# Optimization experiments

Measured on AMD Instinct MI355X. Metric: run time of the kernel, lower is better.

The kernel has to match this reference:

```python
import jax, jax.numpy as jnp
import numpy as np

NUM_NODES = 32768  # B*N = 16*2048
NUM_REL = 10
NUM_BASES = 4
D = 256
E = 524288


def _rgcn_layer(x, src, dst, rel, basis, comp, root, bias):
    """Basis-decomposed relational GCN layer with per-relation mean aggregation.
    x: [N, Din], basis: [NB, Din, Dout], comp: [R, NB], root: [Din, Dout], bias: [Dout].
    """
    n = x.shape[0]
    # project all nodes through each basis once: [N, NB, Dout]
    xb = jnp.einsum('ni,bio->nbo', x, basis)
    coeff = comp[rel]  # [E, NB] per-edge basis coefficients
    # mean normalization per (destination node, relation) pair
    seg = rel * n + dst  # combined segment id, [E]
    cnt = jax.ops.segment_sum(jnp.ones(rel.shape[0], x.dtype), seg,
                              num_segments=NUM_REL * n)
    inv = jnp.where(cnt > 0, 1.0 / cnt, 0.0)[seg]  # [E]
    # per-edge message: sum_b coeff[e,b] * xb[src_e, b, :] (loop over small NB)
    msg = jnp.zeros((rel.shape[0], basis.shape[2]), x.dtype)
    for b in range(basis.shape[0]):
        msg = msg + coeff[:, b:b + 1] * xb[src, b]
    msg = msg * inv[:, None]
    agg = jax.ops.segment_sum(msg, dst, num_segments=n)  # [N, Dout]
    return agg + x @ root + bias


def setup_inputs() -> dict:
    key = jax.random.key(0)
    ks = jax.random.split(key, 16)
    p = lambda k, shp: (jax.random.normal(k, shp, jnp.float32) * 0.05)
    inp = {
        'x': jax.random.normal(ks[0], (16, 2048, D), jnp.float32),
        't': jax.random.randint(ks[1], (16,), 0, 1000),
        'obj_cond': jax.random.randint(ks[2], (16, 2048), 0, 160),
        'edge_cond': jax.random.randint(ks[3], (2, E), 0, NUM_NODES),
        'relation_cond': jax.random.randint(ks[4], (E,), 0, NUM_REL),
        # layer 0: 256 -> 256 (hidden)
        'basis0': p(ks[5], (NUM_BASES, D, D)),
        'comp0': p(ks[6], (NUM_REL, NUM_BASES)),
        'root0': p(ks[7], (D, D)),
        'bias0': p(ks[8], (D,)),
        # layer 1: 256 -> 256 (output)
        'basis1': p(ks[9], (NUM_BASES, D, D)),
        'comp1': p(ks[10], (NUM_REL, NUM_BASES)),
        'root1': p(ks[11], (D, D)),
        'bias1': p(ks[12], (D,)),
    }
    return inp


def reference(x, t, obj_cond, edge_cond, relation_cond,
              basis0, comp0, root0, bias0, basis1, comp1, root1, bias1):
    B, N, Dm = x.shape
    h = x.reshape(B * N, Dm)
    src, dst = edge_cond[0], edge_cond[1]
    h = _rgcn_layer(h, src, dst, relation_cond, basis0, comp0, root0, bias0)
    h = jax.nn.relu(h)  # hidden-layer activation (dropout disabled at eval)
    h = _rgcn_layer(h, src, dst, relation_cond, basis1, comp1, root1, bias1)
    return h.reshape(B, N, Dm)
```

## Files before the change

kernel.cpp:

```cpp
#include <hip/hip_runtime.h>
#include <stdint.h>

#define NNODES 32768
#define NREL 10
#define NBASES 4
#define DIM 256
#define NEDGE 524288
#define KW 1280
#define KBASE 1024

#define HB 2048
#define CB 8192
#define WB 80

typedef __attribute__((ext_vector_type(8))) short bf16x8;
typedef __attribute__((ext_vector_type(4))) float f32x4;
typedef __attribute__((ext_vector_type(2))) float f32x2;

__device__ __forceinline__ float bf2f(unsigned short u){
  union { unsigned int i; float f; } v; v.i = ((unsigned int)u) << 16; return v.f;
}
__device__ __forceinline__ float asf(unsigned int u){
  union { unsigned int i; float f; } v; v.i = u; return v.f;
}
__device__ __forceinline__ unsigned short f2bf(float f){
  union { float f; unsigned int i; } v; v.f = f;
  unsigned int x = v.i;
  unsigned int r = (x + 0x7FFFu + ((x >> 16) & 1u)) >> 16;
  return (unsigned short)r;
}
__device__ __forceinline__ void gll16(const void* g, void* l){
  __builtin_amdgcn_global_load_lds((const __attribute__((address_space(1))) void*)g,
                                   (__attribute__((address_space(3))) void*)l, 16, 0, 0);
}

__global__ __launch_bounds__(256) void mega_prep(
    const int* __restrict__ ec, const int* __restrict__ rel,
    int* __restrict__ cnt_rd,
    const float* __restrict__ x, unsigned short* __restrict__ Xh,
    const float* __restrict__ basis0, const float* __restrict__ root0,
    unsigned short* __restrict__ Wt0,
    const float* __restrict__ basis1, const float* __restrict__ root1,
    unsigned short* __restrict__ Wt1)
{
  __shared__ float tile[64][65];
  int bid = blockIdx.x;
  int t = threadIdx.x;
  if (bid < HB){
    int e = bid * 256 + t;
    int d = ec[NEDGE + e];
    int r = rel[e];
    atomicAdd(&cnt_rd[(r << 15) + d], 1);
  } else if (bid < HB + CB){
    int i = (bid - HB) * 256 + t;
    float4 v = ((const float4*)x)[i];
    ushort4 o; o.x = f2bf(v.x); o.y = f2bf(v.y); o.z = f2bf(v.z); o.w = f2bf(v.w);
    ((ushort4*)Xh)[i] = o;
  } else {
    int b = bid - HB - CB;
    int layer = b / WB; b %= WB;
    const float* basis = layer ? basis1 : basis0;
    const float* root  = layer ? root1  : root0;
    unsigned short* Wt = layer ? Wt1    : Wt0;
    int k0 = (b % 20) * 64;
    int n0 = (b / 20) * 64;
    int tn = t & 63, tk = t >> 6;
#pragma unroll
    for (int i = 0; i < 64; i += 4){
      int k = k0 + tk + i;
      float v = (k < KBASE) ? basis[(size_t)k * 256 + n0 + tn]
                            : root[(size_t)(k - KBASE) * 256 + n0 + tn];
      tile[tk + i][tn] = v;
    }
    __syncthreads();
#pragma unroll
    for (int i = 0; i < 64; i += 4){
      int n = n0 + tk + i;
      Wt[(size_t)n * KW + k0 + tn] = f2bf(tile[tn][tk + i]);
    }
  }
}

__global__ __launch_bounds__(1024) void scan1(const int* __restrict__ cnt_rd,
                                              int* __restrict__ offs, int* __restrict__ blksum)
{
  __shared__ int sh[1024];
  int tid = threadIdx.x; int gid = blockIdx.x * 1024 + tid;
  int v = 0;
#pragma unroll
  for (int r = 0; r < NREL; r++) v += cnt_rd[(r << 15) + gid];
  sh[tid] = v; __syncthreads();
  for (int off = 1; off < 1024; off <<= 1){
    int t = (tid >= off) ? sh[tid - off] : 0;
    __syncthreads(); sh[tid] += t; __syncthreads();
  }
  offs[gid] = sh[tid] - v;
  if (tid == 1023) blksum[blockIdx.x] = sh[1023];
}
__global__ __launch_bounds__(64) void scan2(int* __restrict__ blksum)
{
  __shared__ int sh[64];
  int tid = threadIdx.x;
  int v = (tid < NNODES / 1024) ? blksum[tid] : 0;
  sh[tid] = v; __syncthreads();
  for (int off = 1; off < 64; off <<= 1){
    int t = (tid >= off) ? sh[tid - off] : 0;
    __syncthreads(); sh[tid] += t; __syncthreads();
  }
  if (tid < NNODES / 1024) blksum[tid] = sh[tid] - v;
}
__global__ __launch_bounds__(1024) void scan3(int* __restrict__ offs, const int* __restrict__ blksum)
{
  int gid = blockIdx.x * 1024 + threadIdx.x;
  offs[gid] += blksum[blockIdx.x];
  if (gid == 0) offs[NNODES] = NEDGE;
}

__global__ void scatter_kernel(const int* __restrict__ ec, const int* __restrict__ rel,
                               const int* __restrict__ offs, int* __restrict__ cursor,
                               unsigned int* __restrict__ meta)
{
  int e = blockIdx.x * 256 + threadIdx.x;
  int s = ec[e];
  int d = ec[NEDGE + e];
  int r = rel[e];
  int p = offs[d] + atomicAdd(&cursor[d], 1);
  meta[p] = ((unsigned int)s << 4) | (unsigned int)r;
}

__global__ __launch_bounds__(256) void agg8(
    const unsigned short* __restrict__ Xin,
    const int* __restrict__ offs,
    const unsigned int* __restrict__ meta,
    const float* __restrict__ comp,
    const int* __restrict__ cnt_rd,
    unsigned short* __restrict__ z)
{
  __shared__ __attribute__((aligned(16))) float wtab[4][40];
  int t = threadIdx.x;
  int wv = t >> 6, lane = t & 63;
  int d = blockIdx.x * 4 + wv;
  if (lane < 40){
    int r = lane >> 2, b = lane & 3;
    int cnt = cnt_rd[(r << 15) + d];
    wtab[wv][lane] = (cnt > 0) ? comp[r * NBASES + b] / (float)cnt : 0.0f;
  }
  __syncthreads();

  const float4* wt4 = (const float4*)&wtab[wv][0];
  const char* Xb = (const char*)Xin;
  unsigned colb = (unsigned)(lane * 8);

  f32x2 acc[NBASES][2];
#pragma unroll
  for (int b = 0; b < NBASES; b++){ acc[b][0] = (f32x2){0.f,0.f}; acc[b][1] = (f32x2){0.f,0.f}; }

  int e0 = offs[d], e1 = offs[d + 1];
  int e = e0;

  for (; e + 7 < e1; e += 8){
    unsigned int m[8];
#pragma unroll
    for (int i = 0; i < 8; i++) m[i] = meta[e + i];
    uint2 v[8];
#pragma unroll
    for (int i = 0; i < 8; i++){
      unsigned off = ((m[i] & 0xFFFFFFF0u) << 5) + colb;
      v[i] = *(const uint2*)(Xb + off);
    }
#pragma unroll
    for (int i = 0; i < 8; i++){
      float4 w = wt4[m[i] & 15u];
      f32x2 f01, f23;
      f01.x = asf(v[i].x << 16); f01.y = asf(v[i].x & 0xffff0000u);
      f23.x = asf(v[i].y << 16); f23.y = asf(v[i].y & 0xffff0000u);
      acc[0][0] += (f32x2){w.x, w.x} * f01;  acc[0][1] += (f32x2){w.x, w.x} * f23;
      acc[1][0] += (f32x2){w.y, w.y} * f01;  acc[1][1] += (f32x2){w.y, w.y} * f23;
      acc[2][0] += (f32x2){w.z, w.z} * f01;  acc[2][1] += (f32x2){w.z, w.z} * f23;
      acc[3][0] += (f32x2){w.w, w.w} * f01;  acc[3][1] += (f32x2){w.w, w.w} * f23;
    }
  }

  for (; e < e1; e += 4){
    unsigned int m[4];
    float4 w[4];
#pragma unroll
    for (int i = 0; i < 4; i++){
      int ei = e + i;
      bool ok = ei < e1;
      m[i] = meta[ok ? ei : e1 - 1];
      float4 ww = wt4[m[i] & 15u];
      if (!ok){ ww.x = 0.f; ww.y = 0.f; ww.z = 0.f; ww.w = 0.f; }
      w[i] = ww;
    }
    uint2 v[4];
#pragma unroll
    for (int i = 0; i < 4; i++){
      unsigned off = ((m[i] & 0xFFFFFFF0u) << 5) + colb;
      v[i] = *(const uint2*)(Xb + off);
    }
#pragma unroll
    for (int i = 0; i < 4; i++){
      f32x2 f01, f23;
      f01.x = asf(v[i].x << 16); f01.y = asf(v[i].x & 0xffff0000u);
      f23.x = asf(v[i].y << 16); f23.y = asf(v[i].y & 0xffff0000u);
      acc[0][0] += (f32x2){w[i].x, w[i].x} * f01;  acc[0][1] += (f32x2){w[i].x, w[i].x} * f23;
      acc[1][0] += (f32x2){w[i].y, w[i].y} * f01;  acc[1][1] += (f32x2){w[i].y, w[i].y} * f23;
      acc[2][0] += (f32x2){w[i].z, w[i].z} * f01;  acc[2][1] += (f32x2){w[i].z, w[i].z} * f23;
      acc[3][0] += (f32x2){w[i].w, w[i].w} * f01;  acc[3][1] += (f32x2){w[i].w, w[i].w} * f23;
    }
  }

#pragma unroll
  for (int b = 0; b < NBASES; b++){
    ushort4 o;
    o.x = f2bf(acc[b][0].x); o.y = f2bf(acc[b][0].y);
    o.z = f2bf(acc[b][1].x); o.w = f2bf(acc[b][1].y);
    *(ushort4*)(z + (size_t)d * KBASE + b * 256 + lane * 4) = o;
  }
}

__global__ __launch_bounds__(256) void gemm4(
    const unsigned short* __restrict__ A0,
    const unsigned short* __restrict__ A1,
    const unsigned short* __restrict__ Wt,
    const float* __restrict__ bias,
    unsigned short* __restrict__ outh,
    float* __restrict__ outf,
    int mode)
{
  __shared__ __attribute__((aligned(16))) short As[64 * 32];
  __shared__ __attribute__((aligned(16))) short Bs[256 * 32];
  int tid  = threadIdx.x;
  int m0   = blockIdx.x * 64;
  int lane = tid & 63;
  int wn   = tid >> 6;
  int lq = lane >> 4, lr = lane & 15;

  f32x4 zero = {0.f, 0.f, 0.f, 0.f};
  f32x4 acc[4][4];
#pragma unroll
  for (int i = 0; i < 4; i++)
#pragma unroll
    for (int j = 0; j < 4; j++) acc[i][j] = zero;

  int arow = tid >> 2;
  int akc  = ((tid & 3) - (tid >> 3)) & 3;

  for (int k0 = 0; k0 < KW; k0 += 32){
    __syncthreads();
    {
      const unsigned short* ga;
      if (k0 < KBASE) ga = A0 + (size_t)(m0 + arow) * KBASE + k0 + akc * 8;
      else            ga = A1 + (size_t)(m0 + arow) * 256 + (k0 - KBASE) + akc * 8;
      gll16(ga, As + tid * 8);
    }
#pragma unroll
    for (int i = 0; i < 4; i++){
      int gb  = tid + i * 256;
      int row = gb >> 2;
      int kc  = ((gb & 3) - (gb >> 3)) & 3;
      gll16(Wt + (size_t)row * KW + k0 + kc * 8, Bs + gb * 8);
    }
    __syncthreads();

    bf16x8 af[4], bfr[4];
#pragma unroll
    for (int i = 0; i < 4; i++){
      int row = i * 16 + lr;
      af[i] = *(const bf16x8*)(As + row * 32 + (((lq + (row >> 1)) & 3) * 8));
    }
#pragma unroll
    for (int j = 0; j < 4; j++){
      int row = wn * 64 + j * 16 + lr;
      bfr[j] = *(const bf16x8*)(Bs + row * 32 + (((lq + (row >> 1)) & 3) * 8));
    }
#pragma unroll
    for (int i = 0; i < 4; i++)
#pragma unroll
      for (int j = 0; j < 4; j++)
        acc[i][j] = __builtin_amdgcn_mfma_f32_16x16x32_bf16(af[i], bfr[j], acc[i][j], 0, 0, 0);
  }

#pragma unroll
  for (int i = 0; i < 4; i++)
#pragma unroll
    for (int j = 0; j < 4; j++)
#pragma unroll
      for (int r = 0; r < 4; r++){
        int gm = m0 + i * 16 + lq * 4 + r;
        int gn = wn * 64 + j * 16 + lr;
        float v = acc[i][j][r] + bias[gn];
        size_t idx = (size_t)gm * 256 + gn;
        if (mode == 1) outh[idx] = f2bf(fmaxf(v, 0.f));
        else           outf[idx] = v;
      }
}

extern "C" void kernel_launch(void* const* d_in, const int* in_sizes, int n_in,
                              void* d_out, int out_size, void* d_ws, size_t ws_size,
                              hipStream_t stream)
{
  const float* x      = (const float*)d_in[0];
  const int*   ec     = (const int*)d_in[3];
  const int*   rel    = (const int*)d_in[4];
  const float* basis0 = (const float*)d_in[5];
  const float* comp0  = (const float*)d_in[6];
  const float* root0  = (const float*)d_in[7];
  const float* bias0  = (const float*)d_in[8];
  const float* basis1 = (const float*)d_in[9];
  const float* comp1  = (const float*)d_in[10];
  const float* root1  = (const float*)d_in[11];
  const float* bias1  = (const float*)d_in[12];

  char* p = (char*)d_ws;
  unsigned short* z   = (unsigned short*)p; p += (size_t)NNODES * KBASE * 2;
  unsigned short* Xh  = (unsigned short*)p; p += (size_t)NNODES * DIM * 2;
  unsigned short* h   = (unsigned short*)p; p += (size_t)NNODES * DIM * 2;
  unsigned short* Wt0 = (unsigned short*)p; p += (size_t)256 * KW * 2;
  unsigned short* Wt1 = (unsigned short*)p; p += (size_t)256 * KW * 2;
  unsigned int* meta  = (unsigned int*)p;   p += (size_t)NEDGE * 4;
  int* cnt_rd  = (int*)p;   p += (size_t)NREL * NNODES * 4;
  int* cursor  = (int*)p;   p += (size_t)NNODES * 4;
  int* offs    = (int*)p;   p += (size_t)(NNODES + 1) * 4;
  int* blksum  = (int*)p;   p += 1024;

  hipMemsetAsync(cnt_rd, 0, ((size_t)NREL * NNODES + (size_t)NNODES) * 4, stream);

  mega_prep<<<HB + CB + 2 * WB, 256, 0, stream>>>(
      ec, rel, cnt_rd, x, Xh, basis0, root0, Wt0, basis1, root1, Wt1);

  scan1<<<NNODES / 1024, 1024, 0, stream>>>(cnt_rd, offs, blksum);
  scan2<<<1, 64, 0, stream>>>(blksum);
  scan3<<<NNODES / 1024, 1024, 0, stream>>>(offs, blksum);
  scatter_kernel<<<NEDGE / 256, 256, 0, stream>>>(ec, rel, offs, cursor, meta);

  agg8<<<NNODES / 4, 256, 0, stream>>>(Xh, offs, meta, comp0, cnt_rd, z);
  gemm4<<<NNODES / 64, 256, 0, stream>>>(z, Xh, Wt0, bias0, h, nullptr, 1);

  agg8<<<NNODES / 4, 256, 0, stream>>>(h, offs, meta, comp1, cnt_rd, z);
  gemm4<<<NNODES / 64, 256, 0, stream>>>(z, h, Wt1, bias1, nullptr, (float*)d_out, 2);
}
```

Baseline: 322.8 us.

## Load GEMM weight fragments directly to registers and merge scan passes

After: 352.0 us. +9.1%, slower.

```diff
diff --git a/kernel.cpp b/kernel.cpp
--- a/kernel.cpp
+++ b/kernel.cpp
@@ -97,22 +97,19 @@
   offs[gid] = sh[tid] - v;
   if (tid == 1023) blksum[blockIdx.x] = sh[1023];
 }
-__global__ __launch_bounds__(64) void scan2(int* __restrict__ blksum)
-{
-  __shared__ int sh[64];
-  int tid = threadIdx.x;
-  int v = (tid < NNODES / 1024) ? blksum[tid] : 0;
-  sh[tid] = v; __syncthreads();
-  for (int off = 1; off < 64; off <<= 1){
-    int t = (tid >= off) ? sh[tid - off] : 0;
-    __syncthreads(); sh[tid] += t; __syncthreads();
-  }
-  if (tid < NNODES / 1024) blksum[tid] = sh[tid] - v;
-}
-__global__ __launch_bounds__(1024) void scan3(int* __restrict__ offs, const int* __restrict__ blksum)
-{
-  int gid = blockIdx.x * 1024 + threadIdx.x;
-  offs[gid] += blksum[blockIdx.x];
+__global__ __launch_bounds__(1024) void scan3b(int* __restrict__ offs, const int* __restrict__ blksum)
+{
+  __shared__ int pre;
+  int bid = blockIdx.x;
+  if (threadIdx.x < 64){
+    int v = ((int)threadIdx.x < bid && threadIdx.x < 32) ? blksum[threadIdx.x] : 0;
+#pragma unroll
+    for (int o = 1; o < 64; o <<= 1) v += __shfl_xor(v, o);
+    if (threadIdx.x == 0) pre = v;
+  }
+  __syncthreads();
+  int gid = bid * 1024 + threadIdx.x;
+  offs[gid] += pre;
   if (gid == 0) offs[NNODES] = NEDGE;
 }
 
@@ -220,7 +217,7 @@
   }
 }
 
-__global__ __launch_bounds__(256) void gemm4(
+__global__ __launch_bounds__(256) void gemm8(
     const unsigned short* __restrict__ A0,
     const unsigned short* __restrict__ A1,
     const unsigned short* __restrict__ Wt,
@@ -229,8 +226,7 @@
     float* __restrict__ outf,
     int mode)
 {
-  __shared__ __attribute__((aligned(16))) short As[64 * 32];
-  __shared__ __attribute__((aligned(16))) short Bs[256 * 32];
+  __shared__ __attribute__((aligned(16))) short As[64 * 64];
   int tid  = threadIdx.x;
   int m0   = blockIdx.x * 64;
   int lane = tid & 63;
@@ -244,42 +240,56 @@
 #pragma unroll
     for (int j = 0; j < 4; j++) acc[i][j] = zero;
 
-  int arow = tid >> 2;
-  int akc  = ((tid & 3) - (tid >> 3)) & 3;
-
-  for (int k0 = 0; k0 < KW; k0 += 32){
+  int arow0 = tid >> 3;
+  int akc0  = ((tid & 7) - (tid >> 4)) & 7;
+  int g1    = tid + 256;
+  int arow1 = g1 >> 3;
+  int akc1  = ((g1 & 7) - (g1 >> 4)) & 7;
+
+  const unsigned short* wtb[4];
+#pragma unroll
+  for (int j = 0; j < 4; j++)
+    wtb[j] = Wt + (size_t)(wn * 64 + j * 16 + lr) * KW + lq * 8;
+
+  for (int k0 = 0; k0 < KW; k0 += 64){
     __syncthreads();
     {
-      const unsigned short* ga;
-      if (k0 < KBASE) ga = A0 + (size_t)(m0 + arow) * KBASE + k0 + akc * 8;
-      else            ga = A1 + (size_t)(m0 + arow) * 256 + (k0 - KBASE) + akc * 8;
-      gll16(ga, As + tid * 8);
-    }
-#pragma unroll
-    for (int i = 0; i < 4; i++){
-      int gb  = tid + i * 256;
-      int row = gb >> 2;
-      int kc  = ((gb & 3) - (gb >> 3)) & 3;
-      gll16(Wt + (size_t)row * KW + k0 + kc * 8, Bs + gb * 8);
-    }
+      const unsigned short* ga0, *ga1;
+      if (k0 < KBASE){
+        ga0 = A0 + (size_t)(m0 + arow0) * KBASE + k0 + akc0 * 8;
+        ga1 = A0 + (size_t)(m0 + arow1) * KBASE + k0 + akc1 * 8;
+      } else {
+        ga0 = A1 + (size_t)(m0 + arow0) * 256 + (k0 - KBASE) + akc0 * 8;
+        ga1 = A1 + (size_t)(m0 + arow1) * 256 + (k0 - KBASE) + akc1 * 8;
+      }
+      gll16(ga0, As + tid * 8);
+      gll16(ga1, As + (tid + 256) * 8);
+    }
+    bf16x8 bfr[4][2];
+#pragma unroll
+    for (int j = 0; j < 4; j++)
+#pragma unroll
+      for (int s = 0; s < 2; s++)
+        bfr[j][s] = *(const bf16x8*)(wtb[j] + k0 + s * 32);
     __syncthreads();
 
-    bf16x8 af[4], bfr[4];
+    bf16x8 af[4][2];
 #pragma unroll
     for (int i = 0; i < 4; i++){
       int row = i * 16 + lr;
-      af[i] = *(const bf16x8*)(As + row * 32 + (((lq + (row >> 1)) & 3) * 8));
-    }
-#pragma unroll
-    for (int j = 0; j < 4; j++){
-      int row = wn * 64 + j * 16 + lr;
-      bfr[j] = *(const bf16x8*)(Bs + row * 32 + (((lq + (row >> 1)) & 3) * 8));
+#pragma unroll
+      for (int s = 0; s < 2; s++){
+        int slot = ((lq + 4 * s) + (row >> 1)) & 7;
+        af[i][s] = *(const bf16x8*)(As + row * 64 + slot * 8);
+      }
     }
 #pragma unroll
     for (int i = 0; i < 4; i++)
 #pragma unroll
-      for (int j = 0; j < 4; j++)
-        acc[i][j] = __builtin_amdgcn_mfma_f32_16x16x32_bf16(af[i], bfr[j], acc[i][j], 0, 0, 0);
+      for (int j = 0; j < 4; j++){
+        acc[i][j] = __builtin_amdgcn_mfma_f32_16x16x32_bf16(af[i][0], bfr[j][0], acc[i][j], 0, 0, 0);
+        acc[i][j] = __builtin_amdgcn_mfma_f32_16x16x32_bf16(af[i][1], bfr[j][1], acc[i][j], 0, 0, 0);
+      }
   }
 
 #pragma unroll
@@ -331,13 +341,12 @@
       ec, rel, cnt_rd, x, Xh, basis0, root0, Wt0, basis1, root1, Wt1);
 
   scan1<<<NNODES / 1024, 1024, 0, stream>>>(cnt_rd, offs, blksum);
-  scan2<<<1, 64, 0, stream>>>(blksum);
-  scan3<<<NNODES / 1024, 1024, 0, stream>>>(offs, blksum);
+  scan3b<<<NNODES / 1024, 1024, 0, stream>>>(offs, blksum);
   scatter_kernel<<<NEDGE / 256, 256, 0, stream>>>(ec, rel, offs, cursor, meta);
 
   agg8<<<NNODES / 4, 256, 0, stream>>>(Xh, offs, meta, comp0, cnt_rd, z);
-  gemm4<<<NNODES / 64, 256, 0, stream>>>(z, Xh, Wt0, bias0, h, nullptr, 1);
+  gemm8<<<NNODES / 64, 256, 0, stream>>>(z, Xh, Wt0, bias0, h, nullptr, 1);
 
   agg8<<<NNODES / 4, 256, 0, stream>>>(h, offs, meta, comp1, cnt_rd, z);
-  gemm4<<<NNODES / 64, 256, 0, stream>>>(z, h, Wt1, bias1, nullptr, (float*)d_out, 2);
-}
+  gemm8<<<NNODES / 64, 256, 0, stream>>>(z, h, Wt1, bias1, nullptr, (float*)d_out, 2);
+}
```
